# Performance work log

Hardware: AMD Instinct MI355X
Metric: run time of the kernel (lower is better)

Reference implementation:

```python
import jax, jax.numpy as jnp
import numpy as np

N_NODES = 100000
N_EDGES = 1600000
IN_CH = 128
HID = 128
OUT_CH = 64
N_GRAPHS = 256


def setup_inputs() -> dict:
    key = jax.random.key(0)
    ks = jax.random.split(key, 12)
    x = jax.random.normal(ks[0], (N_NODES, IN_CH), dtype=jnp.float32)
    edge_index = jax.random.randint(ks[1], (2, N_EDGES), 0, N_NODES, dtype=jnp.int64)
    batch = jnp.sort(jax.random.randint(ks[2], (N_NODES,), 0, N_GRAPHS, dtype=jnp.int64))
    def glorot(k, shape):
        lim = np.sqrt(6.0 / (shape[0] + shape[1]))
        return jax.random.uniform(k, shape, jnp.float32, -lim, lim)
    w1 = glorot(ks[3], (IN_CH, HID)); b1 = jnp.zeros((HID,), jnp.float32)
    w2 = glorot(ks[4], (HID, HID));   b2 = jnp.zeros((HID,), jnp.float32)
    w3 = glorot(ks[5], (HID, HID));   b3 = jnp.zeros((HID,), jnp.float32)
    w_out = glorot(ks[6], (HID, OUT_CH)); b_out = jnp.zeros((OUT_CH,), jnp.float32)
    return {"x": x, "edge_index": edge_index, "batch": batch,
            "w1": w1, "b1": b1, "w2": w2, "b2": b2, "w3": w3, "b3": b3,
            "w_out": w_out, "b_out": b_out}


def reference(x, edge_index, batch, w1, b1, w2, b2, w3, b3, w_out, b_out):
    N = x.shape[0]
    # GCN normalization with added self-loops (PyG gcn_norm, symmetric):
    loop = jnp.arange(N, dtype=edge_index.dtype)
    src = jnp.concatenate([edge_index[0], loop])  # message source
    dst = jnp.concatenate([edge_index[1], loop])  # aggregate at target
    deg = jax.ops.segment_sum(jnp.ones(src.shape, jnp.float32), dst, num_segments=N)
    dinv = jax.lax.rsqrt(jnp.maximum(deg, 1.0))  # deg >= 1 due to self-loops
    norm = dinv[src] * dinv[dst]  # [E+N]

    def gcn_conv(h, w, b):
        h = h @ w  # transform first (PyG order)
        agg = jax.ops.segment_sum(norm[:, None] * h[src], dst, num_segments=N)
        return agg + b

    # norm module is None, dropout p=0 -> act-only branch, dropout no-op
    h = jax.nn.relu(gcn_conv(x, w1, b1))
    h = jax.nn.relu(gcn_conv(h, w2, b2))
    h = jax.nn.relu(gcn_conv(h, w3, b3))

    # global mean pool over graphs
    cnt = jax.ops.segment_sum(jnp.ones((N,), jnp.float32), batch, num_segments=N_GRAPHS)
    pooled = jax.ops.segment_sum(h, batch, num_segments=N_GRAPHS) / jnp.maximum(cnt, 1.0)[:, None]
    return pooled @ w_out + b_out  # [N_GRAPHS, OUT_CH]
```

## Files before the change

### kernel.cpp

```cpp
#include <hip/hip_runtime.h>
#include <hip/hip_fp16.h>

#define N_NODES 100000
#define N_EDGES 1600000
#define HID 128
#define OUT_CH 64
#define N_GRAPHS 256
#define NSLICE 8
#define SLICE_NODES ((N_NODES + NSLICE - 1) / NSLICE)
#define CAP 64

typedef _Float16 half8 __attribute__((ext_vector_type(8)));
typedef float f32x4 __attribute__((ext_vector_type(4)));

__global__ void k_setup(int* cnt, float* pooled, float* gcnt,
                        const float* __restrict__ w1, const float* __restrict__ w2,
                        const float* __restrict__ w3,
                        __half* __restrict__ wt1, __half* __restrict__ wt2,
                        __half* __restrict__ wt3) {
  int i = blockIdx.x * blockDim.x + threadIdx.x;
  int stride = gridDim.x * blockDim.x;
  for (int t = i; t < N_NODES; t += stride) cnt[t] = 0;
  for (int t = i; t < N_GRAPHS * HID; t += stride) pooled[t] = 0.f;
  for (int t = i; t < N_GRAPHS; t += stride) gcnt[t] = 0.f;
  for (int t = i; t < HID * HID; t += stride) {
    int n = t >> 7, k = t & 127;
    wt1[t] = __float2half(w1[k * HID + n]);
    wt2[t] = __float2half(w2[k * HID + n]);
    wt3[t] = __float2half(w3[k * HID + n]);
  }
}

__global__ __launch_bounds__(256) void k_fill_pad(const int* __restrict__ ei,
                                                  int* __restrict__ cnt,
                                                  int* __restrict__ E4) {
  int slice = blockIdx.x & (NSLICE - 1);
  int lo = slice * SLICE_NODES;
  int hi = min(lo + SLICE_NODES, N_NODES);
  int bi = blockIdx.x >> 3;
  int step = (gridDim.x >> 3) * 256;
  for (int e = bi * 256 + threadIdx.x; e < N_EDGES; e += step) {
    int d = ei[N_EDGES + e];
    if (d >= lo && d < hi) {
      int s = ei[e];
      int p = atomicAdd(&cnt[d], 1);
      if (p < CAP) E4[(size_t)d * CAP + p] = s;
    }
  }
}

__global__ void k_dinv(int* __restrict__ cnt, float* __restrict__ dinv) {
  int i = blockIdx.x * blockDim.x + threadIdx.x;
  if (i < N_NODES) {
    int c = min(cnt[i], CAP);
    cnt[i] = c;
    dinv[i] = rsqrtf((float)c + 1.0f);
  }
}

#define GBM 64
template <bool FP16IN>
__global__ __launch_bounds__(256) void k_gemm(const void* __restrict__ Hv,
                                              const __half* __restrict__ WT,
                                              __half* __restrict__ T) {
  __shared__ __half hs[GBM * HID];
  __shared__ __half ws[HID * HID];
  int tid = threadIdx.x;
  int m0 = blockIdx.x * GBM;

  for (int g = tid; g < GBM * 16; g += 256) {
    int r = g >> 4, kg = g & 15;
    int row = m0 + r;
    half8 h = {};
    if (row < N_NODES) {
      if constexpr (FP16IN) {
        h = *(const half8*)&((const _Float16*)Hv)[(size_t)row * HID + kg * 8];
      } else {
        const float* H = (const float*)Hv;
        float4 f0 = *(const float4*)&H[(size_t)row * HID + kg * 8];
        float4 f1 = *(const float4*)&H[(size_t)row * HID + kg * 8 + 4];
        h[0] = (_Float16)f0.x; h[1] = (_Float16)f0.y; h[2] = (_Float16)f0.z; h[3] = (_Float16)f0.w;
        h[4] = (_Float16)f1.x; h[5] = (_Float16)f1.y; h[6] = (_Float16)f1.z; h[7] = (_Float16)f1.w;
      }
    }
    int byte = (r * HID + kg * 8) * 2;
    byte ^= (r & 7) << 4;
    *(half8*)((char*)hs + byte) = h;
  }
  for (int g = tid; g < HID * 16; g += 256) {
    int n = g >> 4, kg = g & 15;
    half8 h = *(const half8*)&WT[n * HID + kg * 8];
    int byte = (n * HID + kg * 8) * 2;
    byte ^= (n & 7) << 4;
    *(half8*)((char*)ws + byte) = h;
  }
  __syncthreads();

  int w = tid >> 6, l = tid & 63;
  int r = (w << 4) + (l & 15);
  int kq = (l >> 4) << 3;
  f32x4 acc[8] = {};

  #pragma unroll
  for (int kc = 0; kc < HID; kc += 32) {
    int abyte = ((r * HID + kc + kq) * 2) ^ ((r & 7) << 4);
    half8 a = *(const half8*)((char*)hs + abyte);
    #pragma unroll
    for (int nb = 0; nb < 8; ++nb) {
      int n = nb * 16 + (l & 15);
      int bbyte = ((n * HID + kc + kq) * 2) ^ ((n & 7) << 4);
      half8 bfr = *(const half8*)((char*)ws + bbyte);
      acc[nb] = __builtin_amdgcn_mfma_f32_16x16x32_f16(a, bfr, acc[nb], 0, 0, 0);
    }
  }

  __syncthreads();
  #pragma unroll
  for (int nb = 0; nb < 8; ++nb) {
    #pragma unroll
    for (int j = 0; j < 4; ++j) {
      int rr = (w << 4) + ((l >> 4) << 2) + j;
      int cc = nb * 16 + (l & 15);
      int byte = (rr * HID + cc) * 2;
      byte ^= (rr & 7) << 4;
      *(__half*)((char*)hs + byte) = __float2half(acc[nb][j]);
    }
  }
  __syncthreads();
  for (int g = tid; g < GBM * 16; g += 256) {
    int rr = g >> 4, kg = g & 15;
    int byte = (rr * HID + kg * 8) * 2;
    byte ^= (rr & 7) << 4;
    half8 v = *(half8*)((char*)hs + byte);
    int row = m0 + rr;
    if (row < N_NODES)
      *(half8*)&((_Float16*)T)[(size_t)row * HID + kg * 8] = v;
  }
}

__device__ __forceinline__ void acc8(float* acc, uint4 v, float wt) {
  __half2 h0 = *(__half2*)&v.x, h1 = *(__half2*)&v.y;
  __half2 h2 = *(__half2*)&v.z, h3 = *(__half2*)&v.w;
  float2 f0 = __half22float2(h0), f1 = __half22float2(h1);
  float2 f2 = __half22float2(h2), f3 = __half22float2(h3);
  acc[0] += wt * f0.x; acc[1] += wt * f0.y;
  acc[2] += wt * f1.x; acc[3] += wt * f1.y;
  acc[4] += wt * f2.x; acc[5] += wt * f2.y;
  acc[6] += wt * f3.x; acc[7] += wt * f3.y;
}

__global__ __launch_bounds__(256) void k_agg(const __half* __restrict__ T,
                                             const int* __restrict__ cnt,
                                             const int* __restrict__ E4,
                                             const float* __restrict__ dinv,
                                             const float* __restrict__ bias,
                                             __half* __restrict__ Hout) {
  int wid = (blockIdx.x * blockDim.x + threadIdx.x) >> 6;
  int lane = threadIdx.x & 63;
  if (wid >= N_NODES) return;
  int q = lane >> 4;
  int wch = lane & 15;

  float acc[8] = {};
  float dn = dinv[wid];
  {
    uint4 vs = *(const uint4*)(T + (size_t)wid * HID + wch * 8);
    acc8(acc, vs, (q == 0) ? dn * dn : 0.f);
  }
  int deg = cnt[wid];
  const int* row = E4 + (size_t)wid * CAP;
  for (int p = 0; p < deg; p += 16) {
    int i0 = p + q, i1 = p + 4 + q, i2 = p + 8 + q, i3 = p + 12 + q;
    int c0 = min(i0, deg - 1), c1 = min(i1, deg - 1);
    int c2 = min(i2, deg - 1), c3 = min(i3, deg - 1);
    int s0 = row[c0], s1 = row[c1], s2 = row[c2], s3 = row[c3];
    uint4 v0 = *(const uint4*)(T + (size_t)s0 * HID + wch * 8);
    uint4 v1 = *(const uint4*)(T + (size_t)s1 * HID + wch * 8);
    uint4 v2 = *(const uint4*)(T + (size_t)s2 * HID + wch * 8);
    uint4 v3 = *(const uint4*)(T + (size_t)s3 * HID + wch * 8);
    float w0 = (i0 < deg) ? dinv[s0] * dn : 0.f;
    float w1 = (i1 < deg) ? dinv[s1] * dn : 0.f;
    float w2 = (i2 < deg) ? dinv[s2] * dn : 0.f;
    float w3 = (i3 < deg) ? dinv[s3] * dn : 0.f;
    acc8(acc, v0, w0);
    acc8(acc, v1, w1);
    acc8(acc, v2, w2);
    acc8(acc, v3, w3);
  }
  #pragma unroll
  for (int j = 0; j < 8; ++j) {
    acc[j] += __shfl_xor(acc[j], 16, 64);
    acc[j] += __shfl_xor(acc[j], 32, 64);
  }
  if (q == 0) {
    float4 b0 = *(const float4*)(bias + wch * 8);
    float4 b1 = *(const float4*)(bias + wch * 8 + 4);
    __half2 o0 = __floats2half2_rn(fmaxf(acc[0] + b0.x, 0.f), fmaxf(acc[1] + b0.y, 0.f));
    __half2 o1 = __floats2half2_rn(fmaxf(acc[2] + b0.z, 0.f), fmaxf(acc[3] + b0.w, 0.f));
    __half2 o2 = __floats2half2_rn(fmaxf(acc[4] + b1.x, 0.f), fmaxf(acc[5] + b1.y, 0.f));
    __half2 o3 = __floats2half2_rn(fmaxf(acc[6] + b1.z, 0.f), fmaxf(acc[7] + b1.w, 0.f));
    uint4 o;
    o.x = *(unsigned int*)&o0; o.y = *(unsigned int*)&o1;
    o.z = *(unsigned int*)&o2; o.w = *(unsigned int*)&o3;
    *(uint4*)(Hout + (size_t)wid * HID + wch * 8) = o;
  }
}

#define POOL_NODES 64
__global__ __launch_bounds__(256) void k_pool(const __half* __restrict__ H,
                                              const int* __restrict__ batch,
                                              float* __restrict__ pooled,
                                              float* __restrict__ gcnt) {
  int w = threadIdx.x >> 6;
  int l = threadIdx.x & 63;
  int n0 = blockIdx.x * POOL_NODES + w * 16;
  if (n0 >= N_NODES) return;
  int n1 = min(n0 + 16, N_NODES);
  const __half2* H2 = (const __half2*)H;
  float sx = 0.f, sy = 0.f, cntr = 0.f;
  int cur = batch[n0];
  for (int n = n0; n < n1; ++n) {
    int g = batch[n];
    if (g != cur) {
      atomicAdd(&pooled[cur * HID + 2 * l], sx);
      atomicAdd(&pooled[cur * HID + 2 * l + 1], sy);
      if (l == 0) atomicAdd(&gcnt[cur], cntr);
      sx = 0.f; sy = 0.f; cntr = 0.f; cur = g;
    }
    float2 f = __half22float2(H2[(size_t)n * 64 + l]);
    sx += f.x; sy += f.y; cntr += 1.f;
  }
  atomicAdd(&pooled[cur * HID + 2 * l], sx);
  atomicAdd(&pooled[cur * HID + 2 * l + 1], sy);
  if (l == 0) atomicAdd(&gcnt[cur], cntr);
}

__global__ __launch_bounds__(64) void k_out(const float* __restrict__ pooled,
                                            const float* __restrict__ gcnt,
                                            const float* __restrict__ w_out,
                                            const float* __restrict__ b_out,
                                            float* __restrict__ out) {
  int g = blockIdx.x;
  int c = threadIdx.x;
  __shared__ float p[HID];
  float inv = 1.0f / fmaxf(gcnt[g], 1.0f);
  for (int k = c; k < HID; k += 64) p[k] = pooled[g * HID + k] * inv;
  __syncthreads();
  float acc = b_out[c];
  #pragma unroll 8
  for (int k = 0; k < HID; ++k) acc += p[k] * w_out[k * OUT_CH + c];
  out[g * OUT_CH + c] = acc;
}

extern "C" void kernel_launch(void* const* d_in, const int* in_sizes, int n_in,
                              void* d_out, int out_size, void* d_ws, size_t ws_size,
                              hipStream_t stream) {
  const float* x     = (const float*)d_in[0];
  const int*   ei    = (const int*)d_in[1];
  const int*   batch = (const int*)d_in[2];
  const float* w1    = (const float*)d_in[3];
  const float* b1    = (const float*)d_in[4];
  const float* w2    = (const float*)d_in[5];
  const float* b2    = (const float*)d_in[6];
  const float* w3    = (const float*)d_in[7];
  const float* b3    = (const float*)d_in[8];
  const float* w_out = (const float*)d_in[9];
  const float* b_out = (const float*)d_in[10];
  float* out = (float*)d_out;

  char* w = (char*)d_ws;
  auto alloc = [&](size_t bytes) { void* p = (void*)w; w += (bytes + 255) & ~(size_t)255; return p; };
  int*   cnt        = (int*)  alloc((size_t)N_NODES * 4);
  float* dinv       = (float*)alloc((size_t)N_NODES * 4);
  int*   E4         = (int*)  alloc((size_t)N_NODES * CAP * 4);
  __half* wt1       = (__half*)alloc((size_t)HID * HID * 2);
  __half* wt2       = (__half*)alloc((size_t)HID * HID * 2);
  __half* wt3       = (__half*)alloc((size_t)HID * HID * 2);
  __half* T         = (__half*)alloc((size_t)N_NODES * HID * 2);
  __half* Hh        = (__half*)alloc((size_t)N_NODES * HID * 2);
  float* pooled     = (float*)alloc((size_t)N_GRAPHS * HID * 4);
  float* gcnt       = (float*)alloc((size_t)N_GRAPHS * 4);

  const int NB = (N_NODES + 255) / 256;
  const int GB = (N_NODES + GBM - 1) / GBM;
  const int AB = (N_NODES + 3) / 4;
  const int PB = (N_NODES + POOL_NODES - 1) / POOL_NODES;

  k_setup<<<256, 256, 0, stream>>>(cnt, pooled, gcnt, w1, w2, w3, wt1, wt2, wt3);
  k_fill_pad<<<2048, 256, 0, stream>>>(ei, cnt, E4);
  k_dinv<<<NB, 256, 0, stream>>>(cnt, dinv);

  k_gemm<false><<<GB, 256, 0, stream>>>(x, wt1, T);
  k_agg<<<AB, 256, 0, stream>>>(T, cnt, E4, dinv, b1, Hh);
  k_gemm<true><<<GB, 256, 0, stream>>>(Hh, wt2, T);
  k_agg<<<AB, 256, 0, stream>>>(T, cnt, E4, dinv, b2, Hh);
  k_gemm<true><<<GB, 256, 0, stream>>>(Hh, wt3, T);
  k_agg<<<AB, 256, 0, stream>>>(T, cnt, E4, dinv, b3, Hh);

  k_pool<<<PB, 256, 0, stream>>>(Hh, batch, pooled, gcnt);
  k_out<<<N_GRAPHS, 64, 0, stream>>>(pooled, gcnt, w_out, b_out, out);
}
```

Measured before the change: 379.9 us.

## Slice feature matrices by channel groups so aggregation gathers stay cache-resident

```diff
diff --git a/kernel.cpp b/kernel.cpp
--- a/kernel.cpp
+++ b/kernel.cpp
@@ -9,6 +9,7 @@
 #define NSLICE 8
 #define SLICE_NODES ((N_NODES + NSLICE - 1) / NSLICE)
 #define CAP 64
+#define SLICE_HALFS ((size_t)N_NODES * 16)
 
 typedef _Float16 half8 __attribute__((ext_vector_type(8)));
 typedef float f32x4 __attribute__((ext_vector_type(4)));
@@ -74,7 +75,8 @@
     half8 h = {};
     if (row < N_NODES) {
       if constexpr (FP16IN) {
-        h = *(const half8*)&((const _Float16*)Hv)[(size_t)row * HID + kg * 8];
+        const _Float16* Hs = (const _Float16*)Hv;
+        h = *(const half8*)&Hs[(size_t)(kg >> 1) * SLICE_HALFS + (size_t)row * 16 + (kg & 1) * 8];
       } else {
         const float* H = (const float*)Hv;
         float4 f0 = *(const float4*)&H[(size_t)row * HID + kg * 8];
@@ -128,25 +130,14 @@
   }
   __syncthreads();
   for (int g = tid; g < GBM * 16; g += 256) {
-    int rr = g >> 4, kg = g & 15;
+    int rr = g & 63, kg = g >> 6;
     int byte = (rr * HID + kg * 8) * 2;
     byte ^= (rr & 7) << 4;
     half8 v = *(half8*)((char*)hs + byte);
     int row = m0 + rr;
     if (row < N_NODES)
-      *(half8*)&((_Float16*)T)[(size_t)row * HID + kg * 8] = v;
-  }
-}
-
-__device__ __forceinline__ void acc8(float* acc, uint4 v, float wt) {
-  __half2 h0 = *(__half2*)&v.x, h1 = *(__half2*)&v.y;
-  __half2 h2 = *(__half2*)&v.z, h3 = *(__half2*)&v.w;
-  float2 f0 = __half22float2(h0), f1 = __half22float2(h1);
-  float2 f2 = __half22float2(h2), f3 = __half22float2(h3);
-  acc[0] += wt * f0.x; acc[1] += wt * f0.y;
-  acc[2] += wt * f1.x; acc[3] += wt * f1.y;
-  acc[4] += wt * f2.x; acc[5] += wt * f2.y;
-  acc[6] += wt * f3.x; acc[7] += wt * f3.y;
+      *(half8*)&((_Float16*)T)[(size_t)(kg >> 1) * SLICE_HALFS + (size_t)row * 16 + (kg & 1) * 8] = v;
+  }
 }
 
 __global__ __launch_bounds__(256) void k_agg(const __half* __restrict__ T,
@@ -155,54 +146,47 @@
                                              const float* __restrict__ dinv,
                                              const float* __restrict__ bias,
                                              __half* __restrict__ Hout) {
-  int wid = (blockIdx.x * blockDim.x + threadIdx.x) >> 6;
+  int b = blockIdx.x;
+  int s = b & (NSLICE - 1);
+  int node = (b >> 3) * 4 + (threadIdx.x >> 6);
+  if (node >= N_NODES) return;
   int lane = threadIdx.x & 63;
-  if (wid >= N_NODES) return;
-  int q = lane >> 4;
-  int wch = lane & 15;
-
-  float acc[8] = {};
-  float dn = dinv[wid];
+  int slot = lane >> 3;
+  int cl = lane & 7;
+
+  const _Float16* Ts = (const _Float16*)T + (size_t)s * SLICE_HALFS;
+  float dn = dinv[node];
+  float ax = 0.f, ay = 0.f;
   {
-    uint4 vs = *(const uint4*)(T + (size_t)wid * HID + wch * 8);
-    acc8(acc, vs, (q == 0) ? dn * dn : 0.f);
-  }
-  int deg = cnt[wid];
-  const int* row = E4 + (size_t)wid * CAP;
+    unsigned int v = *(const unsigned int*)(Ts + (size_t)node * 16 + cl * 2);
+    float2 f = __half22float2(*(__half2*)&v);
+    float w0 = (slot == 0) ? dn * dn : 0.f;
+    ax += w0 * f.x; ay += w0 * f.y;
+  }
+  int deg = cnt[node];
+  const int* row = E4 + (size_t)node * CAP;
   for (int p = 0; p < deg; p += 16) {
-    int i0 = p + q, i1 = p + 4 + q, i2 = p + 8 + q, i3 = p + 12 + q;
-    int c0 = min(i0, deg - 1), c1 = min(i1, deg - 1);
-    int c2 = min(i2, deg - 1), c3 = min(i3, deg - 1);
-    int s0 = row[c0], s1 = row[c1], s2 = row[c2], s3 = row[c3];
-    uint4 v0 = *(const uint4*)(T + (size_t)s0 * HID + wch * 8);
-    uint4 v1 = *(const uint4*)(T + (size_t)s1 * HID + wch * 8);
-    uint4 v2 = *(const uint4*)(T + (size_t)s2 * HID + wch * 8);
-    uint4 v3 = *(const uint4*)(T + (size_t)s3 * HID + wch * 8);
-    float w0 = (i0 < deg) ? dinv[s0] * dn : 0.f;
-    float w1 = (i1 < deg) ? dinv[s1] * dn : 0.f;
-    float w2 = (i2 < deg) ? dinv[s2] * dn : 0.f;
-    float w3 = (i3 < deg) ? dinv[s3] * dn : 0.f;
-    acc8(acc, v0, w0);
-    acc8(acc, v1, w1);
-    acc8(acc, v2, w2);
-    acc8(acc, v3, w3);
-  }
-  #pragma unroll
-  for (int j = 0; j < 8; ++j) {
-    acc[j] += __shfl_xor(acc[j], 16, 64);
-    acc[j] += __shfl_xor(acc[j], 32, 64);
-  }
-  if (q == 0) {
-    float4 b0 = *(const float4*)(bias + wch * 8);
-    float4 b1 = *(const float4*)(bias + wch * 8 + 4);
-    __half2 o0 = __floats2half2_rn(fmaxf(acc[0] + b0.x, 0.f), fmaxf(acc[1] + b0.y, 0.f));
-    __half2 o1 = __floats2half2_rn(fmaxf(acc[2] + b0.z, 0.f), fmaxf(acc[3] + b0.w, 0.f));
-    __half2 o2 = __floats2half2_rn(fmaxf(acc[4] + b1.x, 0.f), fmaxf(acc[5] + b1.y, 0.f));
-    __half2 o3 = __floats2half2_rn(fmaxf(acc[6] + b1.z, 0.f), fmaxf(acc[7] + b1.w, 0.f));
-    uint4 o;
-    o.x = *(unsigned int*)&o0; o.y = *(unsigned int*)&o1;
-    o.z = *(unsigned int*)&o2; o.w = *(unsigned int*)&o3;
-    *(uint4*)(Hout + (size_t)wid * HID + wch * 8) = o;
+    int iA = p + slot, iB = p + 8 + slot;
+    int cA = min(iA, deg - 1), cB = min(iB, deg - 1);
+    int sA = row[cA], sB = row[cB];
+    unsigned int vA = *(const unsigned int*)(Ts + (size_t)sA * 16 + cl * 2);
+    unsigned int vB = *(const unsigned int*)(Ts + (size_t)sB * 16 + cl * 2);
+    float wA = (iA < deg) ? dinv[sA] * dn : 0.f;
+    float wB = (iB < deg) ? dinv[sB] * dn : 0.f;
+    float2 fA = __half22float2(*(__half2*)&vA);
+    float2 fB = __half22float2(*(__half2*)&vB);
+    ax += wA * fA.x; ay += wA * fA.y;
+    ax += wB * fB.x; ay += wB * fB.y;
+  }
+  ax += __shfl_xor(ax, 8, 64);  ay += __shfl_xor(ay, 8, 64);
+  ax += __shfl_xor(ax, 16, 64); ay += __shfl_xor(ay, 16, 64);
+  ax += __shfl_xor(ax, 32, 64); ay += __shfl_xor(ay, 32, 64);
+  if (slot == 0) {
+    float bx = bias[s * 16 + cl * 2];
+    float by = bias[s * 16 + cl * 2 + 1];
+    __half2 o = __floats2half2_rn(fmaxf(ax + bx, 0.f), fmaxf(ay + by, 0.f));
+    _Float16* Hs = (_Float16*)Hout + (size_t)s * SLICE_HALFS;
+    *(unsigned int*)(Hs + (size_t)node * 16 + cl * 2) = *(unsigned int*)&o;
   }
 }
 
@@ -216,22 +200,25 @@
   int n0 = blockIdx.x * POOL_NODES + w * 16;
   if (n0 >= N_NODES) return;
   int n1 = min(n0 + 16, N_NODES);
-  const __half2* H2 = (const __half2*)H;
+  int sl = l >> 3, off = l & 7;
+  int ch = sl * 16 + off * 2;
+  const _Float16* Hs = (const _Float16*)H + (size_t)sl * SLICE_HALFS;
   float sx = 0.f, sy = 0.f, cntr = 0.f;
   int cur = batch[n0];
   for (int n = n0; n < n1; ++n) {
     int g = batch[n];
     if (g != cur) {
-      atomicAdd(&pooled[cur * HID + 2 * l], sx);
-      atomicAdd(&pooled[cur * HID + 2 * l + 1], sy);
+      atomicAdd(&pooled[cur * HID + ch], sx);
+      atomicAdd(&pooled[cur * HID + ch + 1], sy);
       if (l == 0) atomicAdd(&gcnt[cur], cntr);
       sx = 0.f; sy = 0.f; cntr = 0.f; cur = g;
     }
-    float2 f = __half22float2(H2[(size_t)n * 64 + l]);
+    unsigned int v = *(const unsigned int*)(Hs + (size_t)n * 16 + off * 2);
+    float2 f = __half22float2(*(__half2*)&v);
     sx += f.x; sy += f.y; cntr += 1.f;
   }
-  atomicAdd(&pooled[cur * HID + 2 * l], sx);
-  atomicAdd(&pooled[cur * HID + 2 * l + 1], sy);
+  atomicAdd(&pooled[cur * HID + ch], sx);
+  atomicAdd(&pooled[cur * HID + ch + 1], sy);
   if (l == 0) atomicAdd(&gcnt[cur], cntr);
 }
 
@@ -283,7 +270,7 @@
 
   const int NB = (N_NODES + 255) / 256;
   const int GB = (N_NODES + GBM - 1) / GBM;
-  const int AB = (N_NODES + 3) / 4;
+  const int AB = (N_NODES / 4) * NSLICE;
   const int PB = (N_NODES + POOL_NODES - 1) / POOL_NODES;
 
   k_setup<<<256, 256, 0, stream>>>(cnt, pooled, gcnt, w1, w2, w3, wt1, wt2, wt3);
```

New measurement: 902.8 us. +137.6%, slower.
